# Optimization experiments

Hardware: AMD Instinct MI355X
Metric: run time of the kernel (lower is better)

Reference implementation:

```python
import jax, jax.numpy as jnp
import numpy as np

B, C3, Dz, H, W = 2, 128, 32, 24, 24
C2, K = 96, 8
E, NH = 256, 4
HD = E // NH
BETA_ADJ = 0.5
EPS = 1e-5
TOPO_HIDDEN = 64


def setup_inputs() -> dict:
    key = jax.random.key(0)
    ks = jax.random.split(key, 10)
    def n(k, shape, s=0.02):
        return jax.random.normal(k, shape, jnp.float32) * s
    return {
        "F3": jax.random.normal(ks[0], (B, C3, Dz, H, W), jnp.float32),
        "F2": jax.random.normal(ks[1], (B, C2, H, W, K), jnp.float32),
        "Wq": n(ks[2], (C3, E)),
        "Wk": n(ks[3], (C2, E)),
        "Wv": n(ks[4], (C2, E)),
        "Wp": n(ks[5], (E, C3)),
        "ln_q_g": jnp.ones((E,), jnp.float32),
        "ln_q_b": jnp.zeros((E,), jnp.float32),
        "ln_kv_g": jnp.ones((E,), jnp.float32),
        "ln_kv_b": jnp.zeros((E,), jnp.float32),
        "conv1_w": n(ks[6], (TOPO_HIDDEN, C2, 3, 3)),
        "bn_g": jnp.ones((TOPO_HIDDEN,), jnp.float32),
        "bn_b": jnp.zeros((TOPO_HIDDEN,), jnp.float32),
        "conv2_w": n(ks[7], (1, TOPO_HIDDEN, 1, 1)),
        "conv2_b": jnp.zeros((1,), jnp.float32),
        "lam": jnp.asarray(0.3, jnp.float32),
        "D0": 128,
        "slab": 16,
    }


def _layernorm(x, g, b):
    m = jnp.mean(x, -1, keepdims=True)
    v = jnp.mean(jnp.square(x - m), -1, keepdims=True)
    return (x - m) * jax.lax.rsqrt(v + EPS) * g + b


def _conv2d(x, w, pad):
    return jax.lax.conv_general_dilated(
        x, w, (1, 1), [(pad, pad), (pad, pad)],
        dimension_numbers=("NCHW", "OIHW", "NCHW"))


def _forward(F3, F2, Wq, Wk, Wv, Wp, ln_q_g, ln_q_b, ln_kv_g, ln_kv_b,
             conv1_w, bn_g, bn_b, conv2_w, conv2_b, lam, D0, slab):
    HW = H * W
    # static slab-index map (D0, slab are Python ints)
    z0 = np.round(np.linspace(0.0, D0 - 1, Dz)).astype(np.int64)
    k_index = np.clip(z0 // slab, 0, K - 1)

    # ---- TopoPriorHead2D (BatchNorm in eval mode, default running stats 0/1) ----
    f2_bkchw = jnp.transpose(F2, (0, 4, 1, 2, 3)).reshape(B * K, C2, H, W)
    h = _conv2d(f2_bkchw, conv1_w, 1)
    h = h * (bn_g / np.float32(np.sqrt(1.0 + EPS)))[None, :, None, None] + bn_b[None, :, None, None]
    h = jax.nn.relu(h)
    p_pred = _conv2d(h, conv2_w, 0) + conv2_b[None, :, None, None]  # [B*K,1,H,W]
    nei = jnp.ones((1, 1, 3, 3), jnp.float32).at[0, 0, 1, 1].set(0.0)
    ps_pred = _conv2d(p_pred, nei, 1)
    topo_map = (p_pred + 0.5 * ps_pred).reshape(B, K, HW)

    # ---- Q/K/V projections + LayerNorm ----
    x2 = jnp.transpose(F2, (0, 4, 2, 3, 1)).reshape(B, K, HW, C2)
    Kall = _layernorm(x2 @ Wk, ln_kv_g, ln_kv_b).reshape(B, K, HW, NH, HD)
    Vall = _layernorm(x2 @ Wv, ln_kv_g, ln_kv_b).reshape(B, K, HW, NH, HD)
    x3 = jnp.transpose(F3, (0, 2, 3, 4, 1)).reshape(B, Dz, HW, C3)
    Qall = _layernorm(x3 @ Wq, ln_q_g, ln_q_b).reshape(B, Dz, HW, NH, HD)

    Oh = jnp.zeros_like(Qall)
    scale = np.float32(1.0 / np.sqrt(HD))
    hw = np.arange(HW)
    for kk in range(K):
        z_ids = np.nonzero(k_index == kk)[0]
        if z_ids.size == 0:
            continue
        cand = [c for c in (kk - 1, kk, kk + 1) if 0 <= c < K]
        L = len(cand)
        slab_bias = jnp.asarray(np.concatenate(
            [np.full(HW, 0.0 if c == kk else -BETA_ADJ, np.float32) for c in cand]))
        Qg = Qall[:, z_ids]                                    # [B,Ds,HW,NH,HD]
        Kc = Kall[:, np.asarray(cand)].reshape(B, L * HW, NH, HD)
        Vc = Vall[:, np.asarray(cand)].reshape(B, L * HW, NH, HD)
        # [B,NH,Ds,HW,M]
        logits = jnp.einsum('bdphc,bmhc->bhdpm', Qg, Kc) * scale
        logits = logits + slab_bias
        # diagonal topo boost: query pixel p attends to same pixel p in slab cand[j]
        diag = jnp.zeros((B, HW, L * HW), logits.dtype)
        for j, c in enumerate(cand):
            diag = diag.at[:, hw, j * HW + hw].add(lam * topo_map[:, c])
        logits = logits + diag[:, None, None]
        attn = jax.nn.softmax(logits, axis=-1)
        Og = jnp.einsum('bhdpm,bmhc->bdphc', attn, Vc)         # [B,Ds,HW,NH,HD]
        Oh = Oh.at[:, z_ids].set(Og)

    Oall = Oh.reshape(B, Dz, HW, E) @ Wp                        # [B,D,HW,C3]
    Oall = jnp.transpose(Oall.reshape(B, Dz, H, W, C3), (0, 4, 1, 2, 3))
    return F3 + Oall


def reference(F3, F2, Wq, Wk, Wv, Wp, ln_q_g, ln_q_b, ln_kv_g, ln_kv_b,
              conv1_w, bn_g, bn_b, conv2_w, conv2_b, lam, D0, slab):
    return _forward(F3, F2, Wq, Wk, Wv, Wp, ln_q_g, ln_q_b, ln_kv_g, ln_kv_b,
                    conv1_w, bn_g, bn_b, conv2_w, conv2_b, lam, D0, slab)
```

## Files before the change

kernel.cpp:

```cpp
#include <hip/hip_runtime.h>

typedef float f32x4 __attribute__((ext_vector_type(4)));
typedef __bf16 bf16x8 __attribute__((ext_vector_type(8)));
typedef unsigned short ushort_t;

#define DEV_INLINE __device__ __forceinline__

constexpr int B_N  = 2;
constexpr int C3_N = 128;
constexpr int C2_N = 96;
constexpr int DZ_N = 32;
constexpr int H_N  = 24;
constexpr int W_N  = 24;
constexpr int K_N  = 8;
constexpr int E_N  = 256;
constexpr int HW_N = 576;

DEV_INLINE unsigned short f2bf(float x) {
  union { __bf16 b; unsigned short u; } v;
  v.b = (__bf16)x;
  return v.u;
}

__global__ __launch_bounds__(384) void pre_conv_pack(
    const float* __restrict__ F2, const float* __restrict__ W1,
    float* __restrict__ Hp,
    const float* __restrict__ Wq, const float* __restrict__ Wk,
    const float* __restrict__ Wv, const float* __restrict__ Wp,
    ushort_t* __restrict__ Wqp, ushort_t* __restrict__ Wkp,
    ushort_t* __restrict__ Wvp, ushort_t* __restrict__ Wpp) {
  __shared__ float simg[8][26][28];
  __shared__ float sw[16 * 97];
  const int bid0 = blockIdx.x;
  if (bid0 >= 256) {
    const int bblk = bid0 - 256, t = threadIdx.x;
    if (t < 256) {
      if (bblk < 256) {
        if (t < 128) Wqp[bblk * 128 + t] = f2bf(Wq[t * 256 + bblk]);
      } else if (bblk < 512) {
        const int n = bblk - 256;
        if (t < 96) Wkp[n * 96 + t] = f2bf(Wk[t * 256 + n]);
      } else if (bblk < 768) {
        const int n = bblk - 512;
        if (t < 96) Wvp[n * 96 + t] = f2bf(Wv[t * 256 + n]);
      } else {
        const int c = bblk - 768;
        Wpp[c * 256 + t] = f2bf(Wp[t * 128 + c]);
      }
    }
    return;
  }
  const int bid = bid0;
  const int cc = bid & 3;
  const int tg = (bid >> 2) & 3;
  const int bk = bid >> 4;
  const int b = bk >> 3, k = bk & 7;
  const int tid = threadIdx.x;
  const int y = tid >> 4;
  const int tq = tid & 15;

  float acc[24];
#pragma unroll
  for (int i = 0; i < 24; i++) acc[i] = 0.f;

  float* simgf = &simg[0][0][0];
  for (int i = tid; i < 8 * 26 * 28; i += 384) simgf[i] = 0.f;
  __syncthreads();

  for (int ch = 0; ch < 3; ch++) {
    if (ch) __syncthreads();
    const int c0 = cc * 24 + ch * 8;
    for (int i = tid; i < 8 * 24 * 24; i += 384) {
      int c = i / 576, p = i - c * 576;
      int yy = p / 24, xx = p - yy * 24;
      simg[c][yy + 1][xx + 1] =
          F2[(((b * C2_N + c0 + c) * H_N + yy) * W_N + xx) * K_N + k];
    }
    for (int i = tid; i < 16 * 72; i += 384) {
      int t2 = i / 72, rest = i - t2 * 72;
      int c = rest / 9, q = rest - c * 9;
      sw[t2 * 97 + c * 12 + q] =
          W1[(tg * 16 + t2) * (C2_N * 9) + (c0 + c) * 9 + q];
    }
    __syncthreads();
#pragma unroll 1
    for (int c = 0; c < 8; c++) {
      float w[9];
#pragma unroll
      for (int q = 0; q < 9; q++) w[q] = sw[tq * 97 + c * 12 + q];
#pragma unroll
      for (int dy = 0; dy < 3; dy++) {
        float r[28];
#pragma unroll
        for (int g = 0; g < 7; g++)
          *(float4*)&r[g * 4] = *(const float4*)&simg[c][y + dy][g * 4];
#pragma unroll
        for (int dx = 0; dx < 3; dx++) {
          float wv = w[dy * 3 + dx];
#pragma unroll
          for (int xx = 0; xx < 24; xx++)
            acc[xx] = fmaf(wv, r[xx + dx], acc[xx]);
        }
      }
    }
  }
  const int t = tg * 16 + tq;
  float* dst = &Hp[((cc * 16 + bk) * 64 + t) * HW_N + y * 24];
#pragma unroll
  for (int xx = 0; xx < 24; xx++) dst[xx] = acc[xx];
}

__global__ __launch_bounds__(576) void topo_tail(
    const float* __restrict__ Hp, const float* __restrict__ bn_g,
    const float* __restrict__ bn_b, const float* __restrict__ W2,
    const float* __restrict__ b2, float* __restrict__ topo) {
  const int bk = blockIdx.x;
  const int p = threadIdx.x;
  __shared__ float pp[26][28];
  float* ppf = &pp[0][0];
  for (int i = p; i < 26 * 28; i += 576) ppf[i] = 0.f;
  const float inv = rsqrtf(1.0f + 1e-5f);
  float acc = b2[0];
#pragma unroll 1
  for (int t = 0; t < 64; t++) {
    float v = 0.f;
#pragma unroll
    for (int c4 = 0; c4 < 4; c4++)
      v += Hp[((c4 * 16 + bk) * 64 + t) * HW_N + p];
    acc = fmaf(W2[t], fmaxf(fmaf(bn_g[t] * inv, v, bn_b[t]), 0.f), acc);
  }
  __syncthreads();
  pp[p / 24 + 1][p % 24 + 1] = acc;
  __syncthreads();
  const int yy = p / 24 + 1, xx = p % 24 + 1;
  float s = pp[yy-1][xx-1] + pp[yy-1][xx] + pp[yy-1][xx+1]
          + pp[yy][xx-1]                  + pp[yy][xx+1]
          + pp[yy+1][xx-1] + pp[yy+1][xx] + pp[yy+1][xx+1];
  topo[bk * HW_N + p] = acc + 0.5f * s;
}

__global__ __launch_bounds__(256) void proj_all(
    const float* __restrict__ F3, const float* __restrict__ F2,
    const ushort_t* __restrict__ Wqp, const ushort_t* __restrict__ Wkp,
    const ushort_t* __restrict__ Wvp,
    ushort_t* __restrict__ Qbf, ushort_t* __restrict__ Kpk,
    ushort_t* __restrict__ Vtp,
    const float* __restrict__ ln_q_g, const float* __restrict__ ln_q_b,
    const float* __restrict__ ln_kv_g, const float* __restrict__ ln_kv_b) {
  __shared__ ushort_t sA[64 * 128];
  __shared__ ushort_t sT[64][264];
  const int tid = threadIdx.x;

  if (blockIdx.x < 144) {
    const int rowG = blockIdx.x * 64;
    {
      const int r = tid & 63, kg = tid >> 6;
      const int rr = rowG + r;
      const int b2 = rr / (K_N * HW_N);
      const int rem = rr - b2 * (K_N * HW_N);
      const int k = rem / HW_N;
      const int p = rem - k * HW_N;
      const float* s0 = F2 + (size_t)b2 * (C2_N * HW_N * K_N) + k + p * K_N;
#pragma unroll
      for (int i = 0; i < 24; i += 2) {
        const int kk = kg * 24 + i;
        const float x0 = s0[kk * (HW_N * K_N)];
        const float x1 = s0[(kk + 1) * (HW_N * K_N)];
        const unsigned pr = (unsigned)f2bf(x0) | ((unsigned)f2bf(x1) << 16);
        ((unsigned*)sA)[r * 64 + (((kk >> 3) + r) & 15) * 4 + ((kk & 7) >> 1)] = pr;
      }
    }
    __syncthreads();
    const int wv = tid >> 6, lane = tid & 63;
    const int quad = lane >> 4, col = lane & 15;
    const int m = wv * 16 + col;
    bf16x8 xb[3];
#pragma unroll
    for (int ks = 0; ks < 3; ks++)
      xb[ks] = *(const bf16x8*)&sA[m * 128 + (((ks * 4 + quad) + m) & 15) * 8];

    const int mrow = rowG + m;
    const int bk = mrow / HW_N;
    const int p = mrow - bk * HW_N;
    const int pc = p >> 6, mm = p & 63;

    {
      f32x4 acc[16];
#pragma unroll
      for (int nt = 0; nt < 16; nt++) {
        const ushort_t* wrow = Wkp + (nt * 16 + col) * 96 + quad * 8;
        f32x4 a = (f32x4){0.f, 0.f, 0.f, 0.f};
#pragma unroll
        for (int ks = 0; ks < 3; ks++) {
          bf16x8 wf = *(const bf16x8*)&wrow[ks * 32];
          a = __builtin_amdgcn_mfma_f32_16x16x32_bf16(wf, xb[ks], a, 0, 0, 0);
        }
        acc[nt] = a;
      }
      float s = 0.f;
#pragma unroll
      for (int nt = 0; nt < 16; nt++)
        s += acc[nt][0] + acc[nt][1] + acc[nt][2] + acc[nt][3];
      s += __shfl_xor(s, 16); s += __shfl_xor(s, 32);
      const float mean = s * (1.f / 256.f);
      float v = 0.f;
#pragma unroll
      for (int nt = 0; nt < 16; nt++)
#pragma unroll
        for (int r = 0; r < 4; r++) {
          const float d = acc[nt][r] - mean;
          v += d * d;
        }
      v += __shfl_xor(v, 16); v += __shfl_xor(v, 32);
      const float rstd = rsqrtf(v * (1.f / 256.f) + 1e-5f);
#pragma unroll
      for (int nt = 0; nt < 16; nt++) {
        const int n0 = nt * 16 + quad * 4;
        const float4 gv = *(const float4*)&ln_kv_g[n0];
        const float4 bv = *(const float4*)&ln_kv_b[n0];
        ushort4 o;
        o.x = f2bf(fmaf((acc[nt][0] - mean) * rstd, gv.x, bv.x));
        o.y = f2bf(fmaf((acc[nt][1] - mean) * rstd, gv.y, bv.y));
        o.z = f2bf(fmaf((acc[nt][2] - mean) * rstd, gv.z, bv.z));
        o.w = f2bf(fmaf((acc[nt][3] - mean) * rstd, gv.w, bv.w));
        const int h = nt >> 2;
        const int grp = ((nt & 3) * 2 + (quad >> 1)) ^ (mm & 7);
        ushort_t* dst = Kpk +
            ((size_t)((bk * 4 + h) * 9 + pc)) * 4096 +
            mm * 64 + grp * 8 + (quad & 1) * 4;
        *(ushort4*)dst = o;
      }
    }

    {
      f32x4 acc[16];
#pragma unroll
      for (int nt = 0; nt < 16; nt++) {
        const ushort_t* wrow = Wvp + (nt * 16 + col) * 96 + quad * 8;
        f32x4 a = (f32x4){0.f, 0.f, 0.f, 0.f};
#pragma unroll
        for (int ks = 0; ks < 3; ks++) {
          bf16x8 wf = *(const bf16x8*)&wrow[ks * 32];
          a = __builtin_amdgcn_mfma_f32_16x16x32_bf16(wf, xb[ks], a, 0, 0, 0);
        }
        acc[nt] = a;
      }
      float s = 0.f;
#pragma unroll
      for (int nt = 0; nt < 16; nt++)
        s += acc[nt][0] + acc[nt][1] + acc[nt][2] + acc[nt][3];
      s += __shfl_xor(s, 16); s += __shfl_xor(s, 32);
      const float mean = s * (1.f / 256.f);
      float v = 0.f;
#pragma unroll
      for (int nt = 0; nt < 16; nt++)
#pragma unroll
        for (int r = 0; r < 4; r++) {
          const float d = acc[nt][r] - mean;
          v += d * d;
        }
      v += __shfl_xor(v, 16); v += __shfl_xor(v, 32);
      const float rstd = rsqrtf(v * (1.f / 256.f) + 1e-5f);
#pragma unroll
      for (int nt = 0; nt < 16; nt++) {
        const int n0 = nt * 16 + quad * 4;
        const float4 gv = *(const float4*)&ln_kv_g[n0];
        const float4 bv = *(const float4*)&ln_kv_b[n0];
        ushort4 o;
        o.x = f2bf(fmaf((acc[nt][0] - mean) * rstd, gv.x, bv.x));
        o.y = f2bf(fmaf((acc[nt][1] - mean) * rstd, gv.y, bv.y));
        o.z = f2bf(fmaf((acc[nt][2] - mean) * rstd, gv.z, bv.z));
        o.w = f2bf(fmaf((acc[nt][3] - mean) * rstd, gv.w, bv.w));
        *(ushort4*)&sT[m][n0] = o;
      }
    }
    __syncthreads();
    const int hh = tid >> 6, d = tid & 63;
    __attribute__((aligned(16))) ushort_t tmp[64];
#pragma unroll
    for (int k = 0; k < 64; k++) {
      const int pk = (k & 32) + ((k & 4) << 2) + ((k & 24) >> 1) + (k & 3);
      tmp[k] = sT[pk][hh * 64 + d];
    }
    const int chunk = (bk * 4 + hh) * 9 + pc;
    uint4* dst = (uint4*)&Vtp[chunk * 4096 + d * 64];
    const int sw = d & 7;
#pragma unroll
    for (int gg = 0; gg < 8; gg++) dst[gg ^ sw] = ((const uint4*)tmp)[gg];
  } else {
    const int rowG = (blockIdx.x - 144) * 64;
    {
      const int r = tid & 63, kg = tid >> 6;
      const int rr = rowG + r;
      const int b2 = rr / (DZ_N * HW_N);
      const int rem = rr - b2 * (DZ_N * HW_N);
      const int o = rem / HW_N;
      const int p = rem - o * HW_N;
      const float* s0 = F3 + (size_t)b2 * (C3_N * DZ_N * HW_N) + o * HW_N + p;
#pragma unroll
      for (int i = 0; i < 32; i += 2) {
        const int k = kg * 32 + i;
        const float x0 = s0[(size_t)k * (DZ_N * HW_N)];
        const float x1 = s0[(size_t)(k + 1) * (DZ_N * HW_N)];
        const unsigned pr = (unsigned)f2bf(x0) | ((unsigned)f2bf(x1) << 16);
        ((unsigned*)sA)[r * 64 + (((k >> 3) + r) & 15) * 4 + ((k & 7) >> 1)] = pr;
      }
    }
    __syncthreads();
    const int wv = tid >> 6, lane = tid & 63;
    const int quad = lane >> 4, col = lane & 15;
    const int m = wv * 16 + col;
    bf16x8 xb[4];
#pragma unroll
    for (int ks = 0; ks < 4; ks++)
      xb[ks] = *(const bf16x8*)&sA[m * 128 + (((ks * 4 + quad) + m) & 15) * 8];
    f32x4 acc[16];
#pragma unroll
    for (int nt = 0; nt < 16; nt++) {
      const ushort_t* wrow = Wqp + (nt * 16 + col) * 128 + quad * 8;
      f32x4 a = (f32x4){0.f, 0.f, 0.f, 0.f};
#pragma unroll
      for (int ks = 0; ks < 4; ks++) {
        bf16x8 wf = *(const bf16x8*)&wrow[ks * 32];
        a = __builtin_amdgcn_mfma_f32_16x16x32_bf16(wf, xb[ks], a, 0, 0, 0);
      }
      acc[nt] = a;
    }
    const int mrow = rowG + m;
    float s = 0.f;
#pragma unroll
    for (int nt = 0; nt < 16; nt++)
      s += acc[nt][0] + acc[nt][1] + acc[nt][2] + acc[nt][3];
    s += __shfl_xor(s, 16); s += __shfl_xor(s, 32);
    const float mean = s * (1.f / 256.f);
    float v = 0.f;
#pragma unroll
    for (int nt = 0; nt < 16; nt++)
#pragma unroll
      for (int r = 0; r < 4; r++) {
        const float d = acc[nt][r] - mean;
        v += d * d;
      }
    v += __shfl_xor(v, 16); v += __shfl_xor(v, 32);
    const float rstd = rsqrtf(v * (1.f / 256.f) + 1e-5f);
    const float QS = 0.18033688f;
    ushort_t* dst = Qbf + (size_t)mrow * E_N;
#pragma unroll
    for (int nt = 0; nt < 16; nt++) {
      const int n0 = nt * 16 + quad * 4;
      const float4 gv = *(const float4*)&ln_q_g[n0];
      const float4 bv = *(const float4*)&ln_q_b[n0];
      ushort4 o;
      o.x = f2bf(QS * fmaf((acc[nt][0] - mean) * rstd, gv.x, bv.x));
      o.y = f2bf(QS * fmaf((acc[nt][1] - mean) * rstd, gv.y, bv.y));
      o.z = f2bf(QS * fmaf((acc[nt][2] - mean) * rstd, gv.z, bv.z));
      o.w = f2bf(QS * fmaf((acc[nt][3] - mean) * rstd, gv.w, bv.w));
      *(ushort4*)&dst[n0] = o;
    }
  }
}

__global__ __launch_bounds__(256) void attn_kernel(
    const ushort_t* __restrict__ Qbf, const ushort_t* __restrict__ Kpk,
    const ushort_t* __restrict__ Vtp, const float* __restrict__ topo,
    const float* __restrict__ lamp, const int* __restrict__ D0p,
    const int* __restrict__ slabp, ushort_t* __restrict__ Obf) {
  const int bid = blockIdx.x;
  const int hb = bid & 7;
  const int h = hb & 3, b = hb >> 2;
  const int zp = (bid >> 3) & 15;
  const int pb = bid >> 7;
  const int p0 = pb * 64;
  const int tid = threadIdx.x;
  const int w = tid >> 6, lane = tid & 63;
  const int quad = lane >> 4, col = lane & 15;
  const int z = zp * 2 + (w >> 1);
  const int th = w & 1;

  const float LOG2E = 1.44269504f;
  const float lam2 = lamp[0] * LOG2E;
  const int D0 = D0p[0], slab = slabp[0];
  const float step = (float)(D0 - 1) / (float)(DZ_N - 1);

  int kkw, kka, kkb;
  {
    int z0 = (int)floorf(fmaf((float)z, step, 0.5f));
    int kv = z0 / slab;
    kkw = kv < 0 ? 0 : (kv > K_N - 1 ? K_N - 1 : kv);
    int z0a = (int)floorf(fmaf((float)(zp * 2), step, 0.5f));
    int z0b = (int)floorf(fmaf((float)(zp * 2 + 1), step, 0.5f));
    int ka = z0a / slab; ka = ka < 0 ? 0 : (ka > K_N - 1 ? K_N - 1 : ka);
    int kb = z0b / slab; kb = kb < 0 ? 0 : (kb > K_N - 1 ? K_N - 1 : kb);
    kka = ka < kb ? ka : kb;
    kkb = ka < kb ? kb : ka;
  }
  const int c_lo = (kka - 1) < 0 ? 0 : (kka - 1);
  const int c_hi = (kkb + 1) > (K_N - 1) ? (K_N - 1) : (kkb + 1);

  __shared__ ushort_t sKV[2][4096];

  auto issue_fill = [&](int buf, int c, int pc) {
    const size_t cb = ((size_t)(((b * K_N + c) * 4 + h) * 9) + pc) * 4096;
#pragma unroll
    for (int j = 0; j < 2; j++) {
      const int seg = (w << 1) + j;
      const ushort_t* gsrc = Kpk + cb + seg * 512 + lane * 8;
      ushort_t* ldst = &sKV[buf][seg * 512];
      __builtin_amdgcn_global_load_lds(
          (const __attribute__((address_space(1))) void*)gsrc,
          (__attribute__((address_space(3))) void*)ldst, 16, 0, 0);
    }
  };

  union { ushort_t u[8]; bf16x8 v; } uo;
#pragma unroll
  for (int i = 0; i < 8; i++) uo.u[i] = 0x3F80;
  const bf16x8 vone = uo.v;

  bf16x8 bq[2][2];
  const int qrow0 = (b * DZ_N + z) * HW_N + p0 + th * 32;
#pragma unroll
  for (int t = 0; t < 2; t++) {
    const ushort_t* qp = &Qbf[(qrow0 + t * 16 + col) * E_N + h * 64 + quad * 8];
    bq[t][0] = *(const bf16x8*)qp;
    bq[t][1] = *(const bf16x8*)(qp + 32);
  }

  f32x4 oacc[2][4];
#pragma unroll
  for (int t = 0; t < 2; t++)
#pragma unroll
    for (int dt = 0; dt < 4; dt++) oacc[t][dt] = (f32x4){0.f, 0.f, 0.f, 0.f};
  f32x4 lacc[2];
  lacc[0] = (f32x4){0.f, 0.f, 0.f, 0.f};
  lacc[1] = (f32x4){0.f, 0.f, 0.f, 0.f};

  const int s7 = col & 7;
  const int o1 = (quad ^ s7) * 8;
  const int o2 = ((quad + 4) ^ s7) * 8;

  int buf = 0;
  issue_fill(0, c_lo, 0);

  for (int c = c_lo; c <= c_hi; c++) {
    const bool act = (c >= kkw - 1) && (c <= kkw + 1);
    const float biasE2 = ((c == kkw) ? -20.0f : -20.5f) * LOG2E;
    const f32x4 bias4 = (f32x4){biasE2, biasE2, biasE2, biasE2};
    const float* topoc = &topo[(b * K_N + c) * HW_N + p0];
#pragma unroll 1
    for (int pc = 0; pc < 9; pc++) {
      __syncthreads();
      {
        int pc2 = pc + 1, c2 = c;
        if (pc2 == 9) { pc2 = 0; c2 = c + 1; }
        if (c2 <= c_hi) issue_fill(buf ^ 1, c2, pc2);
      }
      const ushort_t* sKb = &sKV[buf][0];
      buf ^= 1;
      if (!act) continue;

      const ushort_t* gVb =
          Vtp + ((size_t)(((b * K_N + c) * 4 + h) * 9) + pc) * 4096;
      bf16x8 va[4][2];
#pragma unroll
      for (int dt = 0; dt < 4; dt++) {
        const ushort_t* vr = gVb + (dt * 16 + col) * 64;
        va[dt][0] = *(const bf16x8*)(vr + o1);
        va[dt][1] = *(const bf16x8*)(vr + o2);
      }

      bf16x8 ka[4][2];
#pragma unroll
      for (int kt = 0; kt < 4; kt++) {
        const ushort_t* kr = sKb + (kt * 16 + col) * 64;
        ka[kt][0] = *(const bf16x8*)(kr + o1);
        ka[kt][1] = *(const bf16x8*)(kr + o2);
      }

      bf16x8 pfrag[2][2];
#pragma unroll
      for (int t = 0; t < 2; t++) {
        f32x4 sv[4];
#pragma unroll
        for (int kt = 0; kt < 4; kt++) {
          f32x4 acc = __builtin_amdgcn_mfma_f32_16x16x32_bf16(
              ka[kt][0], bq[t][0], bias4, 0, 0, 0);
          acc = __builtin_amdgcn_mfma_f32_16x16x32_bf16(
              ka[kt][1], bq[t][1], acc, 0, 0, 0);
          sv[kt] = acc;
        }
        float xv[4][4];
#pragma unroll
        for (int kt = 0; kt < 4; kt++)
#pragma unroll
          for (int r = 0; r < 4; r++)
            xv[kt][r] = sv[kt][r];
        if (pc == pb) {
          const int ctt = th * 2 + t;
          const float tv2 = lam2 * topoc[th * 32 + t * 16 + col];
          const bool qok = ((col >> 2) == quad);
#pragma unroll
          for (int kt = 0; kt < 4; kt++)
#pragma unroll
            for (int r = 0; r < 4; r++)
              xv[kt][r] += (qok && kt == ctt && (col & 3) == r) ? tv2 : 0.f;
        }
        float ev[4][4];
#pragma unroll
        for (int kt = 0; kt < 4; kt++)
#pragma unroll
          for (int r = 0; r < 4; r++)
            ev[kt][r] = __builtin_amdgcn_exp2f(xv[kt][r]);
#pragma unroll
        for (int f = 0; f < 2; f++) {
          union { uint4 u; bf16x8 v; } pk;
          pk.u.x = __builtin_amdgcn_perm(__float_as_uint(ev[f*2][1]),
                                         __float_as_uint(ev[f*2][0]), 0x07060302u);
          pk.u.y = __builtin_amdgcn_perm(__float_as_uint(ev[f*2][3]),
                                         __float_as_uint(ev[f*2][2]), 0x07060302u);
          pk.u.z = __builtin_amdgcn_perm(__float_as_uint(ev[f*2+1][1]),
                                         __float_as_uint(ev[f*2+1][0]), 0x07060302u);
          pk.u.w = __builtin_amdgcn_perm(__float_as_uint(ev[f*2+1][3]),
                                         __float_as_uint(ev[f*2+1][2]), 0x07060302u);
          pfrag[t][f] = pk.v;
        }
        lacc[t] = __builtin_amdgcn_mfma_f32_16x16x32_bf16(
            vone, pfrag[t][0], lacc[t], 0, 0, 0);
        lacc[t] = __builtin_amdgcn_mfma_f32_16x16x32_bf16(
            vone, pfrag[t][1], lacc[t], 0, 0, 0);
      }

#pragma unroll
      for (int dt = 0; dt < 4; dt++) {
#pragma unroll
        for (int t = 0; t < 2; t++) {
          oacc[t][dt] = __builtin_amdgcn_mfma_f32_16x16x32_bf16(va[dt][0], pfrag[t][0], oacc[t][dt], 0, 0, 0);
          oacc[t][dt] = __builtin_amdgcn_mfma_f32_16x16x32_bf16(va[dt][1], pfrag[t][1], oacc[t][dt], 0, 0, 0);
        }
      }
    }
  }

#pragma unroll
  for (int t = 0; t < 2; t++) {
    const float invl = 1.f / lacc[t][0];
    const int row = qrow0 + t * 16 + col;
    ushort_t* orow = &Obf[(size_t)row * E_N + h * 64];
#pragma unroll
    for (int dt = 0; dt < 4; dt++) {
      ushort4 o;
      o.x = f2bf(oacc[t][dt][0] * invl);
      o.y = f2bf(oacc[t][dt][1] * invl);
      o.z = f2bf(oacc[t][dt][2] * invl);
      o.w = f2bf(oacc[t][dt][3] * invl);
      *(ushort4*)&orow[dt * 16 + quad * 4] = o;
    }
  }
}

__global__ __launch_bounds__(256) void out_proj_mfma(
    const ushort_t* __restrict__ Obf, const ushort_t* __restrict__ Wpp,
    const float* __restrict__ F3, float* __restrict__ outp) {
  __shared__ float sOut[64][129];
  const int tid = threadIdx.x;
  const int rowG = blockIdx.x * 64;
  const int wv = tid >> 6, lane = tid & 63;
  const int quad = lane >> 4, col = lane & 15;

  const ushort_t* xrow = &Obf[(size_t)(rowG + wv * 16 + col) * E_N + quad * 8];
  bf16x8 af[8];
#pragma unroll
  for (int ks = 0; ks < 8; ks++) af[ks] = *(const bf16x8*)&xrow[ks * 32];

#pragma unroll
  for (int nt = 0; nt < 8; nt++) {
    const ushort_t* wrow = &Wpp[(nt * 16 + col) * 256 + quad * 8];
    f32x4 a = (f32x4){0.f, 0.f, 0.f, 0.f};
#pragma unroll
    for (int ks = 0; ks < 8; ks++) {
      bf16x8 wf = *(const bf16x8*)&wrow[ks * 32];
      a = __builtin_amdgcn_mfma_f32_16x16x32_bf16(af[ks], wf, a, 0, 0, 0);
    }
#pragma unroll
    for (int r = 0; r < 4; r++)
      sOut[wv * 16 + quad * 4 + r][nt * 16 + col] = a[r];
  }
  __syncthreads();
  const int b = rowG / (DZ_N * HW_N);
  const int rem = rowG - b * DZ_N * HW_N;
  const int z = rem / HW_N;
  const int pp0 = rem - z * HW_N;
  const int pl = tid & 63, cg = tid >> 6;
  for (int c = cg * 32; c < cg * 32 + 32; c++) {
    const int gidx = ((b * C3_N + c) * DZ_N + z) * HW_N + pp0 + pl;
    outp[gidx] = F3[gidx] + sOut[pl][c];
  }
}

extern "C" void kernel_launch(void* const* d_in, const int* in_sizes, int n_in,
                              void* d_out, int out_size, void* d_ws, size_t ws_size,
                              hipStream_t stream) {
  (void)in_sizes; (void)n_in; (void)out_size; (void)ws_size;
  const float* F3      = (const float*)d_in[0];
  const float* F2      = (const float*)d_in[1];
  const float* Wq      = (const float*)d_in[2];
  const float* Wk      = (const float*)d_in[3];
  const float* Wv      = (const float*)d_in[4];
  const float* Wp      = (const float*)d_in[5];
  const float* ln_q_g  = (const float*)d_in[6];
  const float* ln_q_b  = (const float*)d_in[7];
  const float* ln_kv_g = (const float*)d_in[8];
  const float* ln_kv_b = (const float*)d_in[9];
  const float* conv1_w = (const float*)d_in[10];
  const float* bn_g    = (const float*)d_in[11];
  const float* bn_b    = (const float*)d_in[12];
  const float* conv2_w = (const float*)d_in[13];
  const float* conv2_b = (const float*)d_in[14];
  const float* lam     = (const float*)d_in[15];
  const int*   D0      = (const int*)d_in[16];
  const int*   slab    = (const int*)d_in[17];
  float* out = (float*)d_out;

  char* ws = (char*)d_ws;
  size_t off = 0;
  auto alloc = [&](size_t bytes) {
    void* p = ws + off;
    off += (bytes + 255) & ~(size_t)255;
    return p;
  };
  const int QROWS = B_N * DZ_N * HW_N;
  const int KVROWS = B_N * K_N * HW_N;
  ushort_t* Qbf = (ushort_t*)alloc((size_t)QROWS * E_N * 2);
  ushort_t* Kpk = (ushort_t*)alloc((size_t)KVROWS * E_N * 2);
  ushort_t* Vtp = (ushort_t*)alloc((size_t)KVROWS * E_N * 2);
  ushort_t* Obf = (ushort_t*)alloc((size_t)QROWS * E_N * 2);
  float* topo = (float*)alloc((size_t)B_N * K_N * HW_N * 4);
  ushort_t* Wqp = (ushort_t*)alloc(256 * 128 * 2);
  ushort_t* Wkp = (ushort_t*)alloc(256 * 96 * 2);
  ushort_t* Wvp = (ushort_t*)alloc(256 * 96 * 2);
  ushort_t* Wpp = (ushort_t*)alloc(128 * 256 * 2);
  float* Hp = (float*)Obf;

  pre_conv_pack<<<1152, 384, 0, stream>>>(
      F2, conv1_w, Hp, Wq, Wk, Wv, Wp, Wqp, Wkp, Wvp, Wpp);
  topo_tail<<<16, 576, 0, stream>>>(Hp, bn_g, bn_b, conv2_w, conv2_b, topo);
  proj_all<<<720, 256, 0, stream>>>(
      F3, F2, Wqp, Wkp, Wvp, Qbf, Kpk, Vtp,
      ln_q_g, ln_q_b, ln_kv_g, ln_kv_b);
  attn_kernel<<<1152, 256, 0, stream>>>(
      Qbf, Kpk, Vtp, topo, lam, D0, slab, Obf);
  out_proj_mfma<<<QROWS / 64, 256, 0, stream>>>(Obf, Wpp, F3, out);
}
```

Before: 315.0 us.

## Fold topo tail into projection kernel and hoist V global loads earlier

The separate topo_tail launch is removed. Its work now runs as 16 extra blocks of proj_all, each using 256 threads over three passes per block, which saves one kernel launch and its serialization. In the attention kernel, the global V fragment loads are moved ahead of the next K/V fill issue and placed behind a sched_barrier, so their latency overlaps the fill and the K loads from LDS. The trade-off is that the topo blocks do serial work with fewer threads and may add to the tail of proj_all, and the hoisted loads raise register pressure.

Result: no change. 319.7 us (+1.5%).

```diff
diff --git a/kernel.cpp b/kernel.cpp
--- a/kernel.cpp
+++ b/kernel.cpp
@@ -110,35 +110,6 @@
   for (int xx = 0; xx < 24; xx++) dst[xx] = acc[xx];
 }
 
-__global__ __launch_bounds__(576) void topo_tail(
-    const float* __restrict__ Hp, const float* __restrict__ bn_g,
-    const float* __restrict__ bn_b, const float* __restrict__ W2,
-    const float* __restrict__ b2, float* __restrict__ topo) {
-  const int bk = blockIdx.x;
-  const int p = threadIdx.x;
-  __shared__ float pp[26][28];
-  float* ppf = &pp[0][0];
-  for (int i = p; i < 26 * 28; i += 576) ppf[i] = 0.f;
-  const float inv = rsqrtf(1.0f + 1e-5f);
-  float acc = b2[0];
-#pragma unroll 1
-  for (int t = 0; t < 64; t++) {
-    float v = 0.f;
-#pragma unroll
-    for (int c4 = 0; c4 < 4; c4++)
-      v += Hp[((c4 * 16 + bk) * 64 + t) * HW_N + p];
-    acc = fmaf(W2[t], fmaxf(fmaf(bn_g[t] * inv, v, bn_b[t]), 0.f), acc);
-  }
-  __syncthreads();
-  pp[p / 24 + 1][p % 24 + 1] = acc;
-  __syncthreads();
-  const int yy = p / 24 + 1, xx = p % 24 + 1;
-  float s = pp[yy-1][xx-1] + pp[yy-1][xx] + pp[yy-1][xx+1]
-          + pp[yy][xx-1]                  + pp[yy][xx+1]
-          + pp[yy+1][xx-1] + pp[yy+1][xx] + pp[yy+1][xx+1];
-  topo[bk * HW_N + p] = acc + 0.5f * s;
-}
-
 __global__ __launch_bounds__(256) void proj_all(
     const float* __restrict__ F3, const float* __restrict__ F2,
     const ushort_t* __restrict__ Wqp, const ushort_t* __restrict__ Wkp,
@@ -146,9 +117,13 @@
     ushort_t* __restrict__ Qbf, ushort_t* __restrict__ Kpk,
     ushort_t* __restrict__ Vtp,
     const float* __restrict__ ln_q_g, const float* __restrict__ ln_q_b,
-    const float* __restrict__ ln_kv_g, const float* __restrict__ ln_kv_b) {
+    const float* __restrict__ ln_kv_g, const float* __restrict__ ln_kv_b,
+    const float* __restrict__ Hp, const float* __restrict__ bn_g,
+    const float* __restrict__ bn_b, const float* __restrict__ W2,
+    const float* __restrict__ b2, float* __restrict__ topo) {
   __shared__ ushort_t sA[64 * 128];
   __shared__ ushort_t sT[64][264];
+  __shared__ float pp[26][28];
   const int tid = threadIdx.x;
 
   if (blockIdx.x < 144) {
@@ -156,11 +131,11 @@
     {
       const int r = tid & 63, kg = tid >> 6;
       const int rr = rowG + r;
-      const int b2 = rr / (K_N * HW_N);
-      const int rem = rr - b2 * (K_N * HW_N);
+      const int b2v = rr / (K_N * HW_N);
+      const int rem = rr - b2v * (K_N * HW_N);
       const int k = rem / HW_N;
       const int p = rem - k * HW_N;
-      const float* s0 = F2 + (size_t)b2 * (C2_N * HW_N * K_N) + k + p * K_N;
+      const float* s0 = F2 + (size_t)b2v * (C2_N * HW_N * K_N) + k + p * K_N;
 #pragma unroll
       for (int i = 0; i < 24; i += 2) {
         const int kk = kg * 24 + i;
@@ -287,16 +262,57 @@
     const int sw = d & 7;
 #pragma unroll
     for (int gg = 0; gg < 8; gg++) dst[gg ^ sw] = ((const uint4*)tmp)[gg];
+  } else if (blockIdx.x < 160) {
+    const int bk = blockIdx.x - 144;
+    const float inv = rsqrtf(1.0f + 1e-5f);
+    float* ppf = &pp[0][0];
+    for (int i = tid; i < 26 * 28; i += 256) ppf[i] = 0.f;
+    float accv[3];
+#pragma unroll
+    for (int pass = 0; pass < 3; pass++) {
+      const int p = tid + pass * 256;
+      accv[pass] = b2[0];
+      if (p < HW_N) {
+#pragma unroll 1
+        for (int t = 0; t < 64; t++) {
+          float v = 0.f;
+#pragma unroll
+          for (int c4 = 0; c4 < 4; c4++)
+            v += Hp[((c4 * 16 + bk) * 64 + t) * HW_N + p];
+          accv[pass] =
+              fmaf(W2[t], fmaxf(fmaf(bn_g[t] * inv, v, bn_b[t]), 0.f),
+                   accv[pass]);
+        }
+      }
+    }
+    __syncthreads();
+#pragma unroll
+    for (int pass = 0; pass < 3; pass++) {
+      const int p = tid + pass * 256;
+      if (p < HW_N) pp[p / 24 + 1][p % 24 + 1] = accv[pass];
+    }
+    __syncthreads();
+#pragma unroll
+    for (int pass = 0; pass < 3; pass++) {
+      const int p = tid + pass * 256;
+      if (p < HW_N) {
+        const int yy = p / 24 + 1, xx = p % 24 + 1;
+        float s = pp[yy-1][xx-1] + pp[yy-1][xx] + pp[yy-1][xx+1]
+                + pp[yy][xx-1]                  + pp[yy][xx+1]
+                + pp[yy+1][xx-1] + pp[yy+1][xx] + pp[yy+1][xx+1];
+        topo[bk * HW_N + p] = accv[pass] + 0.5f * s;
+      }
+    }
   } else {
-    const int rowG = (blockIdx.x - 144) * 64;
+    const int rowG = (blockIdx.x - 160) * 64;
     {
       const int r = tid & 63, kg = tid >> 6;
       const int rr = rowG + r;
-      const int b2 = rr / (DZ_N * HW_N);
-      const int rem = rr - b2 * (DZ_N * HW_N);
+      const int b2v = rr / (DZ_N * HW_N);
+      const int rem = rr - b2v * (DZ_N * HW_N);
       const int o = rem / HW_N;
       const int p = rem - o * HW_N;
-      const float* s0 = F3 + (size_t)b2 * (C3_N * DZ_N * HW_N) + o * HW_N + p;
+      const float* s0 = F3 + (size_t)b2v * (C3_N * DZ_N * HW_N) + o * HW_N + p;
 #pragma unroll
       for (int i = 0; i < 32; i += 2) {
         const int k = kg * 32 + i;
@@ -450,6 +466,19 @@
 #pragma unroll 1
     for (int pc = 0; pc < 9; pc++) {
       __syncthreads();
+
+      bf16x8 va[4][2];
+      if (act) {
+        const ushort_t* gVb =
+            Vtp + ((size_t)(((b * K_N + c) * 4 + h) * 9) + pc) * 4096;
+#pragma unroll
+        for (int dt = 0; dt < 4; dt++) {
+          const ushort_t* vr = gVb + (dt * 16 + col) * 64;
+          va[dt][0] = *(const bf16x8*)(vr + o1);
+          va[dt][1] = *(const bf16x8*)(vr + o2);
+        }
+      }
+      __builtin_amdgcn_sched_barrier(0);
       {
         int pc2 = pc + 1, c2 = c;
         if (pc2 == 9) { pc2 = 0; c2 = c + 1; }
@@ -458,16 +487,6 @@
       const ushort_t* sKb = &sKV[buf][0];
       buf ^= 1;
       if (!act) continue;
-
-      const ushort_t* gVb =
-          Vtp + ((size_t)(((b * K_N + c) * 4 + h) * 9) + pc) * 4096;
-      bf16x8 va[4][2];
-#pragma unroll
-      for (int dt = 0; dt < 4; dt++) {
-        const ushort_t* vr = gVb + (dt * 16 + col) * 64;
-        va[dt][0] = *(const bf16x8*)(vr + o1);
-        va[dt][1] = *(const bf16x8*)(vr + o2);
-      }
 
       bf16x8 ka[4][2];
 #pragma unroll
@@ -643,10 +662,10 @@
 
   pre_conv_pack<<<1152, 384, 0, stream>>>(
       F2, conv1_w, Hp, Wq, Wk, Wv, Wp, Wqp, Wkp, Wvp, Wpp);
-  topo_tail<<<16, 576, 0, stream>>>(Hp, bn_g, bn_b, conv2_w, conv2_b, topo);
-  proj_all<<<720, 256, 0, stream>>>(
+  proj_all<<<736, 256, 0, stream>>>(
       F3, F2, Wqp, Wkp, Wvp, Qbf, Kpk, Vtp,
-      ln_q_g, ln_q_b, ln_kv_g, ln_kv_b);
+      ln_q_g, ln_q_b, ln_kv_g, ln_kv_b,
+      Hp, bn_g, bn_b, conv2_w, conv2_b, topo);
   attn_kernel<<<1152, 256, 0, stream>>>(
       Qbf, Kpk, Vtp, topo, lam, D0, slab, Obf);
   out_proj_mfma<<<QROWS / 64, 256, 0, stream>>>(Obf, Wpp, F3, out);
```
